# Kernel optimization log

Hardware: AMD Instinct MI355X
Metric: run time of the kernel (lower is better)

Reference implementation:

```python
import jax, jax.numpy as jnp
import numpy as np

T, HID, NH, NKV, HD = 2048, 4096, 32, 8, 128
L, R = 64, 64            # get_decompose_dim(4096)
EPS = 1e-6
A_BITS, KV_BITS = 8, 4
KV_GROUP = 128
ROPE_THETA = 1000000.0


def _orth(key, n):
    q, _ = jnp.linalg.qr(jax.random.normal(key, (n, n), dtype=jnp.float32))
    return q


def setup_inputs() -> dict:
    key = jax.random.key(0)
    ks = jax.random.split(key, 8)
    return {
        "hidden_states": jax.random.normal(ks[0], (T, HID), dtype=jnp.float32),
        "positions": jnp.arange(T, dtype=jnp.int32),
        "w_qkv": jax.random.normal(ks[1], ((NH + 2 * NKV) * HD, HID), dtype=jnp.float32) * 0.02,
        "w_o": jax.random.normal(ks[2], (HID, NH * HD), dtype=jnp.float32) * 0.02,
        "q_norm_w": jnp.ones((HD,), jnp.float32),
        "k_norm_w": jnp.ones((HD,), jnp.float32),
        "ln_left": _orth(ks[3], L),     # DecomposeTransMatrix left factor (orthogonal)
        "ln_right": _orth(ks[4], R),    # DecomposeTransMatrix right factor
        "o_trans": _orth(ks[5], NH),    # SingleTransMatrix(num_heads)
        "k_trans": _orth(ks[6], HD),    # SingleTransMatrix(head_dim)
    }


def fake_quant_sym(x, bits):
    # per-token (groupsize=-1) symmetric fake quant over last dim
    qmax = 2.0 ** (bits - 1) - 1.0
    scale = jnp.maximum(jnp.max(jnp.abs(x), axis=-1, keepdims=True) / qmax, 1e-8)
    return jnp.clip(jnp.round(x / scale), -qmax - 1.0, qmax) * scale


def fake_quant_group_asym(x, bits, group):
    # asymmetric fake quant over groups of `group` along last dim
    shp = x.shape
    xg = x.reshape(shp[:-1] + (shp[-1] // group, group))
    qmax = 2.0 ** bits - 1.0
    xmin = jnp.minimum(jnp.min(xg, axis=-1, keepdims=True), 0.0)
    xmax = jnp.maximum(jnp.max(xg, axis=-1, keepdims=True), 0.0)
    scale = jnp.maximum((xmax - xmin) / qmax, 1e-8)
    zero = jnp.round(-xmin / scale)
    q = jnp.clip(jnp.round(xg / scale) + zero, 0.0, qmax)
    return ((q - zero) * scale).reshape(shp)


def rmsnorm(x, w):
    var = jnp.mean(x * x, axis=-1, keepdims=True)
    return x * jax.lax.rsqrt(var + EPS) * w


def rope(x, positions):
    # neox-style (rotate halves), full rotary_dim = head_dim; x: [T, H, D]
    half = HD // 2
    inv = 1.0 / (ROPE_THETA ** (jnp.arange(half, dtype=jnp.float32) / half))
    freqs = positions.astype(jnp.float32)[:, None] * inv[None, :]   # [T, half]
    cos = jnp.cos(freqs)[:, None, :]
    sin = jnp.sin(freqs)[:, None, :]
    x1, x2 = x[..., :half], x[..., half:]
    return jnp.concatenate([x1 * cos - x2 * sin, x2 * cos + x1 * sin], axis=-1)


def reference(hidden_states, positions, w_qkv, w_o, q_norm_w, k_norm_w,
              ln_left, ln_right, o_trans, k_trans):
    # --- ln_trans (decomposed rotation, Kronecker structure) ---
    x = hidden_states.reshape(T, L, R)
    x = jnp.einsum('tlr,lL,rR->tLR', x, ln_left, ln_right).reshape(T, HID)
    # --- activation fake quant + fused QKV projection ---
    x = fake_quant_sym(x, A_BITS)
    qkv = x @ w_qkv.T
    q, k, v = jnp.split(qkv, [NH * HD, NH * HD + NKV * HD], axis=-1)
    q = q.reshape(T, NH, HD)
    k = k.reshape(T, NKV, HD)
    v = v.reshape(T, NKV, HD)
    # --- per-head RMSNorm then RoPE ---
    q = rope(rmsnorm(q, q_norm_w), positions)
    k = rope(rmsnorm(k, k_norm_w), positions)
    # --- kcache incoherence rotation: q @ inv(R)^T, k @ R ---
    q = q @ jnp.linalg.inv(k_trans).T
    k = k @ k_trans
    # --- KV-cache fake quant (4-bit asym, group=head_dim) ---
    k = fake_quant_group_asym(k, KV_BITS, KV_GROUP)
    v = fake_quant_group_asym(v, KV_BITS, KV_GROUP)
    # --- causal GQA attention ---
    rep = NH // NKV
    kk = jnp.repeat(k, rep, axis=1)  # [T, NH, HD]
    vv = jnp.repeat(v, rep, axis=1)
    scores = jnp.einsum('thd,shd->hts', q, kk) * (HD ** -0.5)
    causal = jnp.tril(jnp.ones((T, T), dtype=bool))
    scores = jnp.where(causal[None], scores, jnp.float32(-1e30))
    probs = jax.nn.softmax(scores, axis=-1)
    out = jnp.einsum('hts,shd->thd', probs, vv)   # [T, NH, HD]
    # --- o_trans: torch.matmul(M.T, out[t]) mixes across heads ---
    out = jnp.einsum('ji,tjd->tid', o_trans, out).reshape(T, NH * HD)
    # --- output fake quant + o_proj ---
    out = fake_quant_sym(out, A_BITS)
    return out @ w_o.T
```

## Files before the change

kernel.cpp:

```cpp
#include <hip/hip_runtime.h>
#include <math.h>

#define T_TOK 2048
#define HID   4096
#define NH    32
#define NKV   8
#define HD    128
#define QKVD  6144
#define V_OFF 5120

typedef __attribute__((ext_vector_type(8))) short short8;
typedef __attribute__((ext_vector_type(4))) short s4v;
typedef __attribute__((ext_vector_type(4))) float f32x4;

__device__ __forceinline__ unsigned short f2bf(float x) {
  unsigned u = __builtin_bit_cast(unsigned, x);
  u += 0x7fffu + ((u >> 16) & 1u);
  return (unsigned short)(u >> 16);
}
__device__ __forceinline__ float bf2f(unsigned short h) {
  unsigned u = ((unsigned)h) << 16;
  return __builtin_bit_cast(float, u);
}

__device__ __forceinline__ void g2lds16(const void* g, void* l) {
  __builtin_amdgcn_global_load_lds(
      (const __attribute__((address_space(1))) unsigned int*)g,
      (__attribute__((address_space(3))) unsigned int*)(unsigned int)(unsigned long long)l,
      16, 0, 0);
}

__device__ __forceinline__ float wave_sum(float v) {
  for (int off = 32; off; off >>= 1) v += __shfl_xor(v, off, 64);
  return v;
}
__device__ __forceinline__ float wave_max(float v) {
  for (int off = 32; off; off >>= 1) v = fmaxf(v, __shfl_xor(v, off, 64));
  return v;
}
__device__ __forceinline__ float wave_min(float v) {
  for (int off = 32; off; off >>= 1) v = fminf(v, __shfl_xor(v, off, 64));
  return v;
}

__global__ __launch_bounds__(256) void k_f32_to_bf16(
    const float* __restrict__ s, unsigned short* __restrict__ d, int n8)
{
  int i = blockIdx.x * 256 + threadIdx.x;
  if (i >= n8) return;
  const float4* sp = (const float4*)s + (size_t)i * 2;
  float4 a = sp[0], b = sp[1];
  short8 o;
  o[0] = f2bf(a.x); o[1] = f2bf(a.y); o[2] = f2bf(a.z); o[3] = f2bf(a.w);
  o[4] = f2bf(b.x); o[5] = f2bf(b.y); o[6] = f2bf(b.z); o[7] = f2bf(b.w);
  *(short8*)(d + (size_t)i * 8) = o;
}

__global__ __launch_bounds__(256) void k_bilinear_quant(
    const float* __restrict__ hidden, const float* __restrict__ lnL,
    const float* __restrict__ lnR, unsigned short* __restrict__ xqb,
    float* __restrict__ scales)
{
  __shared__ float sX[4096];
  __shared__ float sT[4096];
  __shared__ float sL[4096];
  __shared__ float sR[4096];
  __shared__ float sm[4];
  const int t = blockIdx.x;
  const int tid = threadIdx.x;
  const float* src = hidden + (size_t)t * 4096;
  for (int i = tid; i < 4096; i += 256) { sX[i] = src[i]; sL[i] = lnL[i]; sR[i] = lnR[i]; }
  __syncthreads();
  #pragma unroll
  for (int u = 0; u < 16; u++) {
    int p = tid + 256 * u;
    int l = p >> 6, R = p & 63;
    float a = 0.f;
    #pragma unroll 8
    for (int r = 0; r < 64; r++) a += sX[(l << 6) + r] * sR[(r << 6) + R];
    sT[p] = a;
  }
  __syncthreads();
  float vals[16];
  float amax = 0.f;
  #pragma unroll
  for (int u = 0; u < 16; u++) {
    int p = tid + 256 * u;
    int L = p >> 6, R = p & 63;
    float a = 0.f;
    #pragma unroll 8
    for (int l = 0; l < 64; l++) a += sL[(l << 6) + L] * sT[(l << 6) + R];
    vals[u] = a;
    amax = fmaxf(amax, fabsf(a));
  }
  amax = wave_max(amax);
  if ((tid & 63) == 0) sm[tid >> 6] = amax;
  __syncthreads();
  amax = fmaxf(fmaxf(sm[0], sm[1]), fmaxf(sm[2], sm[3]));
  float scale = fmaxf(amax * (1.0f / 127.0f), 1e-8f);
  if (tid == 0) scales[t] = scale;
  #pragma unroll
  for (int u = 0; u < 16; u++) {
    int p = tid + 256 * u;
    float q = rintf(vals[u] / scale);
    q = fminf(fmaxf(q, -128.f), 127.f);
    xqb[(size_t)t * 4096 + p] = f2bf(q);
  }
}

__global__ __launch_bounds__(256) void k_gemm_split(
    const unsigned short* __restrict__ A, const float* __restrict__ Bf,
    const float* __restrict__ scales, float* __restrict__ C, int N, int K)
{
  __shared__ __align__(16) unsigned short sA[128 * 32];
  __shared__ __align__(16) unsigned short sBh[128 * 32];
  __shared__ __align__(16) unsigned short sBl[128 * 32];
  __shared__ float sS[128];
  const int tid = threadIdx.x;
  const int w = tid >> 6, lane = tid & 63;
  const int n16 = lane & 15, quad = lane >> 4;
  const int bm = blockIdx.y << 7, bn = blockIdx.x << 7;
  const int wm = (w >> 1) << 6, wn = (w & 1) << 6;
  if (tid < 128) sS[tid] = scales[bm + tid];
  const int srow = lane >> 2;
  const int scol = (lane & 3) << 3;
  f32x4 acc[4][4];
  #pragma unroll
  for (int i = 0; i < 4; i++)
    #pragma unroll
    for (int j = 0; j < 4; j++) acc[i][j] = (f32x4){0.f, 0.f, 0.f, 0.f};

  for (int k0 = 0; k0 < K; k0 += 32) {
    __syncthreads();
    #pragma unroll
    for (int r = 0; r < 2; r++) {
      const int grp = (r << 2) + w;
      const int row = (grp << 4) + srow;
      g2lds16(A + (size_t)(bm + row) * K + k0 + scol, &sA[(grp << 9) + lane * 8]);
    }
    #pragma unroll
    for (int it = 0; it < 4; it++) {
      int idx = it * 256 + tid;
      int row = idx >> 3, c4 = (idx & 7) << 2;
      float4 f = *(const float4*)(Bf + (size_t)(bn + row) * K + k0 + c4);
      unsigned short h0 = f2bf(f.x), h1 = f2bf(f.y), h2 = f2bf(f.z), h3 = f2bf(f.w);
      *(s4v*)&sBh[row * 32 + c4] = (s4v){(short)h0, (short)h1, (short)h2, (short)h3};
      *(s4v*)&sBl[row * 32 + c4] = (s4v){
          (short)f2bf(f.x - bf2f(h0)), (short)f2bf(f.y - bf2f(h1)),
          (short)f2bf(f.z - bf2f(h2)), (short)f2bf(f.w - bf2f(h3))};
    }
    __syncthreads();
    short8 af[4], bh[4], bl[4];
    #pragma unroll
    for (int t = 0; t < 4; t++) {
      af[t] = *(const short8*)&sA [(wm + (t << 4) + n16) * 32 + (quad << 3)];
      bh[t] = *(const short8*)&sBh[(wn + (t << 4) + n16) * 32 + (quad << 3)];
      bl[t] = *(const short8*)&sBl[(wn + (t << 4) + n16) * 32 + (quad << 3)];
    }
    #pragma unroll
    for (int i = 0; i < 4; i++)
      #pragma unroll
      for (int j = 0; j < 4; j++) {
        acc[i][j] = __builtin_amdgcn_mfma_f32_16x16x32_bf16(af[i], bh[j], acc[i][j], 0, 0, 0);
        acc[i][j] = __builtin_amdgcn_mfma_f32_16x16x32_bf16(af[i], bl[j], acc[i][j], 0, 0, 0);
      }
  }

  #pragma unroll
  for (int i = 0; i < 4; i++) {
    #pragma unroll
    for (int r = 0; r < 4; r++) {
      int lrow = wm + (i << 4) + (quad << 2) + r;
      float s = sS[lrow];
      float* crow = C + (size_t)(bm + lrow) * N + bn + wn;
      #pragma unroll
      for (int j = 0; j < 4; j++)
        crow[(j << 4) + n16] = acc[i][j][r] * s;
    }
  }
}

__global__ __launch_bounds__(256) void k_gemm_mfma(
    const unsigned short* __restrict__ A, const unsigned short* __restrict__ Bm,
    const float* __restrict__ scales, float* __restrict__ C, int N, int K)
{
  __shared__ __align__(16) unsigned short sA[128 * 32];
  __shared__ __align__(16) unsigned short sB[128 * 32];
  __shared__ float sS[128];
  const int tid = threadIdx.x;
  const int w = tid >> 6, lane = tid & 63;
  const int n16 = lane & 15, quad = lane >> 4;
  const int bm = blockIdx.y << 7, bn = blockIdx.x << 7;
  const int wm = (w >> 1) << 6, wn = (w & 1) << 6;
  if (tid < 128) sS[tid] = scales[bm + tid];
  const int srow = lane >> 2;
  const int scol = (lane & 3) << 3;
  f32x4 acc[4][4];
  #pragma unroll
  for (int i = 0; i < 4; i++)
    #pragma unroll
    for (int j = 0; j < 4; j++) acc[i][j] = (f32x4){0.f, 0.f, 0.f, 0.f};

  for (int k0 = 0; k0 < K; k0 += 32) {
    __syncthreads();
    #pragma unroll
    for (int r = 0; r < 2; r++) {
      const int grp = (r << 2) + w;
      const int row = (grp << 4) + srow;
      g2lds16(A  + (size_t)(bm + row) * K + k0 + scol, &sA[(grp << 9) + lane * 8]);
      g2lds16(Bm + (size_t)(bn + row) * K + k0 + scol, &sB[(grp << 9) + lane * 8]);
    }
    __syncthreads();
    short8 af[4], bfr[4];
    #pragma unroll
    for (int t = 0; t < 4; t++) {
      af[t]  = *(const short8*)&sA[(wm + (t << 4) + n16) * 32 + (quad << 3)];
      bfr[t] = *(const short8*)&sB[(wn + (t << 4) + n16) * 32 + (quad << 3)];
    }
    #pragma unroll
    for (int i = 0; i < 4; i++)
      #pragma unroll
      for (int j = 0; j < 4; j++)
        acc[i][j] = __builtin_amdgcn_mfma_f32_16x16x32_bf16(af[i], bfr[j], acc[i][j], 0, 0, 0);
  }

  #pragma unroll
  for (int i = 0; i < 4; i++) {
    #pragma unroll
    for (int r = 0; r < 4; r++) {
      int lrow = wm + (i << 4) + (quad << 2) + r;
      float s = sS[lrow];
      float* crow = C + (size_t)(bm + lrow) * N + bn + wn;
      #pragma unroll
      for (int j = 0; j < 4; j++)
        crow[(j << 4) + n16] = acc[i][j][r] * s;
    }
  }
}

__global__ __launch_bounds__(64) void k_qkproc(
    const float* __restrict__ qkv, const int* __restrict__ pos,
    const float* __restrict__ nw, const float* __restrict__ kt,
    unsigned short* __restrict__ dst_, int nheads, int off_n, int do_quant)
{
  const int h = blockIdx.x, t = blockIdx.y;
  const int lane = threadIdx.x;
  const float* src = qkv + (size_t)t * QKVD + off_n + h * HD;
  float x1 = src[lane], x2 = src[lane + 64];
  float ss = wave_sum(x1 * x1 + x2 * x2);
  float rinv = 1.0f / sqrtf(ss * (1.0f / 128.0f) + 1e-6f);
  x1 *= rinv * nw[lane];
  x2 *= rinv * nw[lane + 64];
  const float p = (float)pos[t];
  const float invf = exp2f((float)lane * (-19.931568569324174f / 64.0f));
  const float fr = p * invf;
  const float c = cosf(fr), s = sinf(fr);
  const float y1 = x1 * c - x2 * s;
  const float y2 = x2 * c + x1 * s;
  __shared__ float sq[128];
  sq[lane] = y1; sq[lane + 64] = y2;
  __syncthreads();
  float o1 = 0.f, o2 = 0.f;
  #pragma unroll 8
  for (int e = 0; e < 128; e++) {
    float qe = sq[e];
    o1 += qe * kt[(e << 7) + lane];
    o2 += qe * kt[(e << 7) + 64 + lane];
  }
  if (do_quant) {
    float mn = fminf(wave_min(fminf(o1, o2)), 0.f);
    float mx = fmaxf(wave_max(fmaxf(o1, o2)), 0.f);
    float scale = fmaxf((mx - mn) * (1.0f / 15.0f), 1e-8f);
    float zero = rintf(-mn / scale);
    float q1 = fminf(fmaxf(rintf(o1 / scale) + zero, 0.f), 15.f);
    float q2 = fminf(fmaxf(rintf(o2 / scale) + zero, 0.f), 15.f);
    o1 = (q1 - zero) * scale;
    o2 = (q2 - zero) * scale;
  }
  unsigned short* d = dst_ + ((size_t)t * nheads + h) * HD;
  d[lane] = f2bf(o1); d[lane + 64] = f2bf(o2);
}

__global__ __launch_bounds__(256) void k_vproc(
    const float* __restrict__ qkv, unsigned short* __restrict__ vpT)
{
  __shared__ __align__(16) unsigned short sTt[128][72];
  const int kvh = blockIdx.x;
  const int t0  = blockIdx.y * 64;
  const int tid = threadIdx.x;
  const int tl = tid >> 2, part = tid & 3;
  const float* src = qkv + (size_t)(t0 + tl) * QKVD + V_OFF + kvh * HD + part * 32;
  float v[32];
  float mn = 0.f, mx = 0.f;
  #pragma unroll
  for (int c = 0; c < 8; c++) {
    float4 f = *(const float4*)(src + c * 4);
    v[c*4+0] = f.x; v[c*4+1] = f.y; v[c*4+2] = f.z; v[c*4+3] = f.w;
    mn = fminf(mn, fminf(fminf(f.x, f.y), fminf(f.z, f.w)));
    mx = fmaxf(mx, fmaxf(fmaxf(f.x, f.y), fmaxf(f.z, f.w)));
  }
  mn = fminf(mn, __shfl_xor(mn, 1, 64)); mn = fminf(mn, __shfl_xor(mn, 2, 64));
  mx = fmaxf(mx, __shfl_xor(mx, 1, 64)); mx = fmaxf(mx, __shfl_xor(mx, 2, 64));
  float scale = fmaxf((mx - mn) * (1.0f / 15.0f), 1e-8f);
  float zero  = rintf(-mn / scale);
  #pragma unroll
  for (int j = 0; j < 32; j++) {
    float q = fminf(fmaxf(rintf(v[j] / scale) + zero, 0.f), 15.f);
    sTt[part * 32 + j][tl] = f2bf((q - zero) * scale);
  }
  __syncthreads();
  for (int i = tid; i < 128 * 8; i += 256) {
    int d = i >> 3, seg = i & 7;
    *(float4*)(vpT + ((size_t)kvh * HD + d) * T_TOK + t0 + seg * 8) =
        *(const float4*)&sTt[d][seg * 8];
  }
}

__global__ __launch_bounds__(256) void k_attn_mfma(
    const unsigned short* __restrict__ qp, const unsigned short* __restrict__ kp,
    const unsigned short* __restrict__ vpT, float* __restrict__ ao)
{
  __shared__ __align__(16) unsigned short sK[64][136];
  __shared__ __align__(16) unsigned short sVt[128][72];
  __shared__ __align__(16) unsigned short sP[4][16][72];
  const int qb = blockIdx.x, h = blockIdx.y;
  const int kvh = h >> 2;
  const int q0 = qb * 64;
  const int tid = threadIdx.x;
  const int w = tid >> 6;
  const int lane = tid & 63;
  const int n = lane & 15;
  const int quad = lane >> 4;

  short8 qfrag[4];
  {
    const unsigned short* qrow = qp + ((size_t)(q0 + w * 16 + n) * NH + h) * HD;
    #pragma unroll
    for (int kk = 0; kk < 4; kk++)
      qfrag[kk] = *(const short8*)(qrow + kk * 32 + quad * 8);
  }

  f32x4 oacc[8];
  #pragma unroll
  for (int dt = 0; dt < 8; dt++) oacc[dt] = (f32x4){0.f, 0.f, 0.f, 0.f};
  float m_i[4], l_i[4];
  #pragma unroll
  for (int r = 0; r < 4; r++) { m_i[r] = -1e30f; l_i[r] = 0.f; }

  const float sm_scale = 0.08838834764831845f;
  const float LOG2E = 1.4426950408889634f;

  for (int s0 = 0; s0 <= q0; s0 += 64) {
    __syncthreads();
    for (int i = tid; i < 1024; i += 256) {
      int row = i >> 4, ch = i & 15;
      *(float4*)&sK[row][ch * 8] =
          *(const float4*)(kp + ((size_t)(s0 + row) * NKV + kvh) * HD + ch * 8);
    }
    for (int i = tid; i < 1024; i += 256) {
      int row = i >> 3, ch = i & 7;
      *(float4*)&sVt[row][ch * 8] =
          *(const float4*)(vpT + ((size_t)kvh * HD + row) * T_TOK + s0 + ch * 8);
    }
    __syncthreads();

    f32x4 sacc[4];
    #pragma unroll
    for (int jt = 0; jt < 4; jt++) {
      f32x4 c = (f32x4){0.f, 0.f, 0.f, 0.f};
      #pragma unroll
      for (int kk = 0; kk < 4; kk++) {
        short8 b = *(const short8*)&sK[jt * 16 + n][kk * 32 + quad * 8];
        c = __builtin_amdgcn_mfma_f32_16x16x32_bf16(qfrag[kk], b, c, 0, 0, 0);
      }
      sacc[jt] = c;
    }

    float mx[4] = {-1e30f, -1e30f, -1e30f, -1e30f};
    #pragma unroll
    for (int jt = 0; jt < 4; jt++) {
      #pragma unroll
      for (int r = 0; r < 4; r++) {
        int sg = s0 + jt * 16 + n;
        int ig = q0 + w * 16 + quad * 4 + r;
        float v = (sg <= ig) ? sacc[jt][r] * sm_scale : -1e30f;
        sacc[jt][r] = v;
        mx[r] = fmaxf(mx[r], v);
      }
    }
    #pragma unroll
    for (int off = 1; off < 16; off <<= 1)
      #pragma unroll
      for (int r = 0; r < 4; r++) mx[r] = fmaxf(mx[r], __shfl_xor(mx[r], off, 64));
    float alpha[4], psum[4];
    #pragma unroll
    for (int r = 0; r < 4; r++) {
      float m_new = fmaxf(m_i[r], mx[r]);
      alpha[r] = exp2f((m_i[r] - m_new) * LOG2E);
      m_i[r] = m_new;
      psum[r] = 0.f;
    }
    #pragma unroll
    for (int jt = 0; jt < 4; jt++) {
      #pragma unroll
      for (int r = 0; r < 4; r++) {
        float pv = exp2f((sacc[jt][r] - m_i[r]) * LOG2E);
        psum[r] += pv;
        sP[w][quad * 4 + r][jt * 16 + n] = f2bf(pv);
      }
    }
    #pragma unroll
    for (int off = 1; off < 16; off <<= 1)
      #pragma unroll
      for (int r = 0; r < 4; r++) psum[r] += __shfl_xor(psum[r], off, 64);
    #pragma unroll
    for (int r = 0; r < 4; r++) l_i[r] = l_i[r] * alpha[r] + psum[r];
    #pragma unroll
    for (int dt = 0; dt < 8; dt++)
      #pragma unroll
      for (int r = 0; r < 4; r++) oacc[dt][r] *= alpha[r];
    __syncthreads();

    short8 pfrag[2];
    #pragma unroll
    for (int kk = 0; kk < 2; kk++)
      pfrag[kk] = *(const short8*)&sP[w][n][kk * 32 + quad * 8];
    #pragma unroll
    for (int dt = 0; dt < 8; dt++) {
      f32x4 c = oacc[dt];
      #pragma unroll
      for (int kk = 0; kk < 2; kk++) {
        short8 b = *(const short8*)&sVt[dt * 16 + n][kk * 32 + quad * 8];
        c = __builtin_amdgcn_mfma_f32_16x16x32_bf16(pfrag[kk], b, c, 0, 0, 0);
      }
      oacc[dt] = c;
    }
  }

  #pragma unroll
  for (int r = 0; r < 4; r++) {
    float linv = 1.0f / l_i[r];
    int t = q0 + w * 16 + quad * 4 + r;
    float* dst = ao + (size_t)t * (NH * HD) + h * HD;
    #pragma unroll
    for (int dt = 0; dt < 8; dt++)
      dst[dt * 16 + n] = oacc[dt][r] * linv;
  }
}

__global__ __launch_bounds__(256) void k_mix_quant(
    const float* __restrict__ ao, const float* __restrict__ ot,
    unsigned short* __restrict__ qob, float* __restrict__ scales)
{
  __shared__ float sA[4096];
  __shared__ float sO[1024];
  __shared__ float sm[4];
  const int t = blockIdx.x;
  const int tid = threadIdx.x;
  for (int i = tid; i < 4096; i += 256) sA[i] = ao[(size_t)t * 4096 + i];
  for (int i = tid; i < 1024; i += 256) sO[i] = ot[i];
  __syncthreads();
  float vals[16];
  float amax = 0.f;
  #pragma unroll
  for (int u = 0; u < 16; u++) {
    int o = tid + 256 * u;
    int ih = o >> 7, d = o & 127;
    float a = 0.f;
    #pragma unroll 8
    for (int j = 0; j < 32; j++) a += sO[j * 32 + ih] * sA[j * 128 + d];
    vals[u] = a;
    amax = fmaxf(amax, fabsf(a));
  }
  amax = wave_max(amax);
  if ((tid & 63) == 0) sm[tid >> 6] = amax;
  __syncthreads();
  amax = fmaxf(fmaxf(sm[0], sm[1]), fmaxf(sm[2], sm[3]));
  float scale = fmaxf(amax * (1.0f / 127.0f), 1e-8f);
  if (tid == 0) scales[t] = scale;
  #pragma unroll
  for (int u = 0; u < 16; u++) {
    int o = tid + 256 * u;
    float q = rintf(vals[u] / scale);
    q = fminf(fmaxf(q, -128.f), 127.f);
    qob[(size_t)t * 4096 + o] = f2bf(q);
  }
}

extern "C" void kernel_launch(void* const* d_in, const int* in_sizes, int n_in,
                              void* d_out, int out_size, void* d_ws, size_t ws_size,
                              hipStream_t stream) {
  const float* hidden    = (const float*)d_in[0];
  const int*   positions = (const int*)  d_in[1];
  const float* w_qkv     = (const float*)d_in[2];
  const float* w_o       = (const float*)d_in[3];
  const float* q_norm_w  = (const float*)d_in[4];
  const float* k_norm_w  = (const float*)d_in[5];
  const float* ln_left   = (const float*)d_in[6];
  const float* ln_right  = (const float*)d_in[7];
  const float* o_trans   = (const float*)d_in[8];
  const float* k_trans   = (const float*)d_in[9];
  float* out = (float*)d_out;
  char* ws = (char*)d_ws;

  float*          qkv  = (float*)(ws);
  unsigned short* xqb  = (unsigned short*)(ws + 50331648);
  float*          sc1  = (float*)(ws + 67108864);
  float*          sc2  = (float*)(ws + 67117056);
  unsigned short* qp   = (unsigned short*)(ws + 67125248);
  unsigned short* kp   = (unsigned short*)(ws + 83902464);
  unsigned short* vpT  = (unsigned short*)(ws + 88096768);
  unsigned short* wob  = (unsigned short*)(ws + 92291072);
  float*          ao   = qkv;
  unsigned short* qob  = xqb;

  k_bilinear_quant<<<T_TOK, 256, 0, stream>>>(hidden, ln_left, ln_right, xqb, sc1);
  k_gemm_split<<<dim3(QKVD / 128, T_TOK / 128), 256, 0, stream>>>(xqb, w_qkv, sc1, qkv, QKVD, HID);
  k_qkproc<<<dim3(NH, T_TOK), 64, 0, stream>>>(qkv, positions, q_norm_w, k_trans, qp, NH, 0, 0);
  k_qkproc<<<dim3(NKV, T_TOK), 64, 0, stream>>>(qkv, positions, k_norm_w, k_trans, kp, NKV, NH * HD, 1);
  k_vproc<<<dim3(NKV, T_TOK / 64), 256, 0, stream>>>(qkv, vpT);
  k_f32_to_bf16<<<(HID * HID / 8 + 255) / 256, 256, 0, stream>>>(w_o, wob, HID * HID / 8);
  k_attn_mfma<<<dim3(T_TOK / 64, NH), 256, 0, stream>>>(qp, kp, vpT, ao);
  k_mix_quant<<<T_TOK, 256, 0, stream>>>(ao, o_trans, qob, sc2);
  k_gemm_mfma<<<dim3(HID / 128, T_TOK / 128), 256, 0, stream>>>(qob, wob, sc2, out, HID, HID);
}
```

Baseline: 1.103 ms.

## Pair causal query tiles per block to balance work and share K/V tiles

The attention kernel now pairs query tile i with tile 31-i, so each block does the same amount of causal work. Each block loads K/V tiles once into shared memory and reuses them for both query tiles' MFMAs, halving the blocks and the shared-memory K/V staging per unit of work. It also applies the causal mask only on diagonal tiles and drops the block barrier before the per-wave P fragments are read. In exchange, each thread holds twice the accumulator and Q-fragment registers, which may reduce occupancy.

Result: slower. 1.147 ms (+4.0%).

```diff
diff --git a/kernel.cpp b/kernel.cpp
--- a/kernel.cpp
+++ b/kernel.cpp
@@ -316,41 +316,45 @@
   }
 }
 
-__global__ __launch_bounds__(256) void k_attn_mfma(
+__global__ __launch_bounds__(256) void k_attn_pair(
     const unsigned short* __restrict__ qp, const unsigned short* __restrict__ kp,
     const unsigned short* __restrict__ vpT, float* __restrict__ ao)
 {
   __shared__ __align__(16) unsigned short sK[64][136];
   __shared__ __align__(16) unsigned short sVt[128][72];
-  __shared__ __align__(16) unsigned short sP[4][16][72];
-  const int qb = blockIdx.x, h = blockIdx.y;
+  __shared__ __align__(16) unsigned short sP[4][2][16][72];
+  const int pi = blockIdx.x, h = blockIdx.y;
   const int kvh = h >> 2;
-  const int q0 = qb * 64;
+  const int tlo = pi, thi = 31 - pi;
   const int tid = threadIdx.x;
-  const int w = tid >> 6;
-  const int lane = tid & 63;
-  const int n = lane & 15;
-  const int quad = lane >> 4;
-
-  short8 qfrag[4];
-  {
-    const unsigned short* qrow = qp + ((size_t)(q0 + w * 16 + n) * NH + h) * HD;
+  const int w = tid >> 6, lane = tid & 63;
+  const int n = lane & 15, quad = lane >> 4;
+  const int q0t[2] = { tlo * 64, thi * 64 };
+
+  short8 qfrag[2][4];
+  #pragma unroll
+  for (int tt = 0; tt < 2; tt++) {
+    const unsigned short* qrow = qp + ((size_t)(q0t[tt] + w * 16 + n) * NH + h) * HD;
     #pragma unroll
     for (int kk = 0; kk < 4; kk++)
-      qfrag[kk] = *(const short8*)(qrow + kk * 32 + quad * 8);
-  }
-
-  f32x4 oacc[8];
-  #pragma unroll
-  for (int dt = 0; dt < 8; dt++) oacc[dt] = (f32x4){0.f, 0.f, 0.f, 0.f};
-  float m_i[4], l_i[4];
-  #pragma unroll
-  for (int r = 0; r < 4; r++) { m_i[r] = -1e30f; l_i[r] = 0.f; }
+      qfrag[tt][kk] = *(const short8*)(qrow + kk * 32 + quad * 8);
+  }
+
+  f32x4 oacc[2][8];
+  float m_i[2][4], l_i[2][4];
+  #pragma unroll
+  for (int tt = 0; tt < 2; tt++) {
+    #pragma unroll
+    for (int dt = 0; dt < 8; dt++) oacc[tt][dt] = (f32x4){0.f, 0.f, 0.f, 0.f};
+    #pragma unroll
+    for (int r = 0; r < 4; r++) { m_i[tt][r] = -1e30f; l_i[tt][r] = 0.f; }
+  }
 
   const float sm_scale = 0.08838834764831845f;
   const float LOG2E = 1.4426950408889634f;
 
-  for (int s0 = 0; s0 <= q0; s0 += 64) {
+  for (int st = 0; st <= thi; st++) {
+    const int s0 = st * 64;
     __syncthreads();
     for (int i = tid; i < 1024; i += 256) {
       int row = i >> 4, ch = i & 15;
@@ -364,87 +368,115 @@
     }
     __syncthreads();
 
-    f32x4 sacc[4];
+    const int act0 = (st <= tlo) ? 0 : 1;
+
+    f32x4 sacc[2][4];
+    #pragma unroll
+    for (int tt = 0; tt < 2; tt++)
+      #pragma unroll
+      for (int jt = 0; jt < 4; jt++) sacc[tt][jt] = (f32x4){0.f, 0.f, 0.f, 0.f};
     #pragma unroll
     for (int jt = 0; jt < 4; jt++) {
-      f32x4 c = (f32x4){0.f, 0.f, 0.f, 0.f};
-      #pragma unroll
-      for (int kk = 0; kk < 4; kk++) {
-        short8 b = *(const short8*)&sK[jt * 16 + n][kk * 32 + quad * 8];
-        c = __builtin_amdgcn_mfma_f32_16x16x32_bf16(qfrag[kk], b, c, 0, 0, 0);
+      short8 bk[4];
+      #pragma unroll
+      for (int kk = 0; kk < 4; kk++)
+        bk[kk] = *(const short8*)&sK[jt * 16 + n][kk * 32 + quad * 8];
+      #pragma unroll
+      for (int tt = 0; tt < 2; tt++) {
+        if (tt < act0) continue;
+        #pragma unroll
+        for (int kk = 0; kk < 4; kk++)
+          sacc[tt][jt] = __builtin_amdgcn_mfma_f32_16x16x32_bf16(qfrag[tt][kk], bk[kk], sacc[tt][jt], 0, 0, 0);
       }
-      sacc[jt] = c;
-    }
-
-    float mx[4] = {-1e30f, -1e30f, -1e30f, -1e30f};
-    #pragma unroll
-    for (int jt = 0; jt < 4; jt++) {
+    }
+
+    #pragma unroll
+    for (int tt = 0; tt < 2; tt++) {
+      if (tt < act0) continue;
+      const bool diag = (st == (tt ? thi : tlo));
+      float mx[4] = {-1e30f, -1e30f, -1e30f, -1e30f};
+      #pragma unroll
+      for (int jt = 0; jt < 4; jt++) {
+        #pragma unroll
+        for (int r = 0; r < 4; r++) {
+          float v = sacc[tt][jt][r] * sm_scale;
+          if (diag) {
+            int sg = s0 + jt * 16 + n;
+            int ig = q0t[tt] + w * 16 + quad * 4 + r;
+            if (sg > ig) v = -1e30f;
+          }
+          sacc[tt][jt][r] = v;
+          mx[r] = fmaxf(mx[r], v);
+        }
+      }
+      #pragma unroll
+      for (int off = 1; off < 16; off <<= 1)
+        #pragma unroll
+        for (int r = 0; r < 4; r++) mx[r] = fmaxf(mx[r], __shfl_xor(mx[r], off, 64));
+      float alpha[4], psum[4];
       #pragma unroll
       for (int r = 0; r < 4; r++) {
-        int sg = s0 + jt * 16 + n;
-        int ig = q0 + w * 16 + quad * 4 + r;
-        float v = (sg <= ig) ? sacc[jt][r] * sm_scale : -1e30f;
-        sacc[jt][r] = v;
-        mx[r] = fmaxf(mx[r], v);
+        float m_new = fmaxf(m_i[tt][r], mx[r]);
+        alpha[r] = exp2f((m_i[tt][r] - m_new) * LOG2E);
+        m_i[tt][r] = m_new;
+        psum[r] = 0.f;
       }
-    }
-    #pragma unroll
-    for (int off = 1; off < 16; off <<= 1)
-      #pragma unroll
-      for (int r = 0; r < 4; r++) mx[r] = fmaxf(mx[r], __shfl_xor(mx[r], off, 64));
-    float alpha[4], psum[4];
+      #pragma unroll
+      for (int jt = 0; jt < 4; jt++) {
+        #pragma unroll
+        for (int r = 0; r < 4; r++) {
+          float pv = exp2f((sacc[tt][jt][r] - m_i[tt][r]) * LOG2E);
+          psum[r] += pv;
+          sP[w][tt][quad * 4 + r][jt * 16 + n] = f2bf(pv);
+        }
+      }
+      #pragma unroll
+      for (int off = 1; off < 16; off <<= 1)
+        #pragma unroll
+        for (int r = 0; r < 4; r++) psum[r] += __shfl_xor(psum[r], off, 64);
+      #pragma unroll
+      for (int r = 0; r < 4; r++) l_i[tt][r] = l_i[tt][r] * alpha[r] + psum[r];
+      #pragma unroll
+      for (int dt = 0; dt < 8; dt++)
+        #pragma unroll
+        for (int r = 0; r < 4; r++) oacc[tt][dt][r] *= alpha[r];
+    }
+
+    short8 pf[2][2];
+    #pragma unroll
+    for (int tt = 0; tt < 2; tt++) {
+      if (tt < act0) continue;
+      #pragma unroll
+      for (int kk = 0; kk < 2; kk++)
+        pf[tt][kk] = *(const short8*)&sP[w][tt][n][kk * 32 + quad * 8];
+    }
+    #pragma unroll
+    for (int dt = 0; dt < 8; dt++) {
+      short8 bv[2];
+      #pragma unroll
+      for (int kk = 0; kk < 2; kk++)
+        bv[kk] = *(const short8*)&sVt[dt * 16 + n][kk * 32 + quad * 8];
+      #pragma unroll
+      for (int tt = 0; tt < 2; tt++) {
+        if (tt < act0) continue;
+        #pragma unroll
+        for (int kk = 0; kk < 2; kk++)
+          oacc[tt][dt] = __builtin_amdgcn_mfma_f32_16x16x32_bf16(pf[tt][kk], bv[kk], oacc[tt][dt], 0, 0, 0);
+      }
+    }
+  }
+
+  #pragma unroll
+  for (int tt = 0; tt < 2; tt++) {
     #pragma unroll
     for (int r = 0; r < 4; r++) {
-      float m_new = fmaxf(m_i[r], mx[r]);
-      alpha[r] = exp2f((m_i[r] - m_new) * LOG2E);
-      m_i[r] = m_new;
-      psum[r] = 0.f;
-    }
-    #pragma unroll
-    for (int jt = 0; jt < 4; jt++) {
-      #pragma unroll
-      for (int r = 0; r < 4; r++) {
-        float pv = exp2f((sacc[jt][r] - m_i[r]) * LOG2E);
-        psum[r] += pv;
-        sP[w][quad * 4 + r][jt * 16 + n] = f2bf(pv);
-      }
-    }
-    #pragma unroll
-    for (int off = 1; off < 16; off <<= 1)
-      #pragma unroll
-      for (int r = 0; r < 4; r++) psum[r] += __shfl_xor(psum[r], off, 64);
-    #pragma unroll
-    for (int r = 0; r < 4; r++) l_i[r] = l_i[r] * alpha[r] + psum[r];
-    #pragma unroll
-    for (int dt = 0; dt < 8; dt++)
-      #pragma unroll
-      for (int r = 0; r < 4; r++) oacc[dt][r] *= alpha[r];
-    __syncthreads();
-
-    short8 pfrag[2];
-    #pragma unroll
-    for (int kk = 0; kk < 2; kk++)
-      pfrag[kk] = *(const short8*)&sP[w][n][kk * 32 + quad * 8];
-    #pragma unroll
-    for (int dt = 0; dt < 8; dt++) {
-      f32x4 c = oacc[dt];
-      #pragma unroll
-      for (int kk = 0; kk < 2; kk++) {
-        short8 b = *(const short8*)&sVt[dt * 16 + n][kk * 32 + quad * 8];
-        c = __builtin_amdgcn_mfma_f32_16x16x32_bf16(pfrag[kk], b, c, 0, 0, 0);
-      }
-      oacc[dt] = c;
-    }
-  }
-
-  #pragma unroll
-  for (int r = 0; r < 4; r++) {
-    float linv = 1.0f / l_i[r];
-    int t = q0 + w * 16 + quad * 4 + r;
-    float* dst = ao + (size_t)t * (NH * HD) + h * HD;
-    #pragma unroll
-    for (int dt = 0; dt < 8; dt++)
-      dst[dt * 16 + n] = oacc[dt][r] * linv;
+      float linv = 1.0f / l_i[tt][r];
+      int t = q0t[tt] + w * 16 + quad * 4 + r;
+      float* dst = ao + (size_t)t * (NH * HD) + h * HD;
+      #pragma unroll
+      for (int dt = 0; dt < 8; dt++)
+        dst[dt * 16 + n] = oacc[tt][dt][r] * linv;
+    }
   }
 }
 
@@ -520,7 +552,7 @@
   k_qkproc<<<dim3(NKV, T_TOK), 64, 0, stream>>>(qkv, positions, k_norm_w, k_trans, kp, NKV, NH * HD, 1);
   k_vproc<<<dim3(NKV, T_TOK / 64), 256, 0, stream>>>(qkv, vpT);
   k_f32_to_bf16<<<(HID * HID / 8 + 255) / 256, 256, 0, stream>>>(w_o, wob, HID * HID / 8);
-  k_attn_mfma<<<dim3(T_TOK / 64, NH), 256, 0, stream>>>(qp, kp, vpT, ao);
+  k_attn_pair<<<dim3(16, NH), 256, 0, stream>>>(qp, kp, vpT, ao);
   k_mix_quant<<<T_TOK, 256, 0, stream>>>(ao, o_trans, qob, sc2);
   k_gemm_mfma<<<dim3(HID / 128, T_TOK / 128), 256, 0, stream>>>(qob, wob, sc2, out, HID, HID);
 }
```
